# Performance work log

Measured on AMD Instinct MI355X. Metric: run time of the kernel, lower is better.

The kernel has to match this reference:

```python
import jax, jax.numpy as jnp
import numpy as np

B, N_NODES, VOCAB, H = 128, 1023, 2048, 256  # depth-9 perfect binary trees (heap layout)


def setup_inputs() -> dict:
    key = jax.random.key(0)
    k1, k2, k3, k4, k5 = jax.random.split(key, 5)
    tokens = jax.random.randint(k1, (B, N_NODES), 0, VOCAB)
    emb = jax.random.normal(k2, (VOCAB, H), dtype=jnp.float32) * 0.02
    Wx = jax.random.normal(k3, (H, 5 * H), dtype=jnp.float32) * 0.02
    Ul = jax.random.normal(k4, (H, 5 * H), dtype=jnp.float32) * 0.02
    Ur = jax.random.normal(k5, (H, 5 * H), dtype=jnp.float32) * 0.02
    b = jnp.zeros((5 * H,), dtype=jnp.float32)
    return {"tokens": tokens, "emb": emb, "Wx": Wx, "Ul": Ul, "Ur": Ur, "b": b}


def _tree_lstm(tokens, emb, Wx, Ul, Ur, b):
    # tokens: [B, 2^(D+1)-1] in level-order heap layout; children of heap index i
    # are 2i+1, 2i+2 -> within level d+1 they sit at offsets 2k, 2k+1.
    n_nodes = tokens.shape[1]
    depth = int(np.log2(n_nodes + 1)) - 1
    hdim = emb.shape[1]
    x_all = emb[tokens]  # [B, N, H] embedding lookup (memory-bound gather)
    h = c = None
    for d in range(depth, -1, -1):  # bottom-up over levels (fixed structural loop)
        start, n = 2 ** d - 1, 2 ** d
        x = x_all[:, start:start + n]  # [B, n, H]
        gates = jnp.einsum('bnh,hg->bng', x, Wx) + b
        if h is not None:
            hl, hr = h[:, 0::2], h[:, 1::2]
            cl, cr = c[:, 0::2], c[:, 1::2]
            gates = gates + jnp.einsum('bnh,hg->bng', hl, Ul) + jnp.einsum('bnh,hg->bng', hr, Ur)
        i, fl, fr, o, u = jnp.split(gates, 5, axis=-1)
        i, fl, fr, o = map(jax.nn.sigmoid, (i, fl, fr, o))
        u = jnp.tanh(u)
        c_new = i * u
        if c is not None:
            c_new = c_new + fl * cl + fr * cr
        c = c_new
        h = o * jnp.tanh(c)
    return h[:, 0], c[:, 0]  # root states, each [B, H]


def reference(tokens, emb, Wx, Ul, Ur, b):
    h_root, _ = _tree_lstm(tokens, emb, Wx, Ul, Ur, b)
    return h_root  # [B, H]
```

## Files before the change

kernel.cpp:

```cpp
#include <hip/hip_runtime.h>
#include <hip/hip_bf16.h>
#include <math.h>

#define B_SZ   128
#define HDIM   256
#define NG     1280
#define NNODES 1023
#define VOCAB  2048

typedef unsigned int uint32;
typedef short  short8v  __attribute__((ext_vector_type(8)));
typedef float  float4v  __attribute__((ext_vector_type(4)));

__device__ __forceinline__ float sigm(float x) {
    return 1.0f / (1.0f + __expf(-x));
}
__device__ __forceinline__ float tanh_fast(float x) {
    return 2.0f / (1.0f + __expf(-2.0f * x)) - 1.0f;
}
__device__ __forceinline__ float bf2f(unsigned short u) {
    return __uint_as_float(((uint32)u) << 16);
}
__device__ __forceinline__ unsigned short f2bf(float f) {
    uint32 x = __float_as_uint(f);
    uint32 r = (x + 0x7FFFu + ((x >> 16) & 1u)) >> 16;
    return (unsigned short)r;
}

__device__ __forceinline__ void dma16(const unsigned short* gptr, unsigned short* lptr) {
    __builtin_amdgcn_global_load_lds(
        (const __attribute__((address_space(1))) void*)gptr,
        (__attribute__((address_space(3))) void*)lptr, 16, 0, 0);
}

__global__ __launch_bounds__(256) void embb_kernel(
    const float* __restrict__ emb, unsigned short* __restrict__ embb)
{
    const int t = blockIdx.x * 256 + threadIdx.x;
    const float4 v0 = *(const float4*)(emb + (size_t)t * 8);
    const float4 v1 = *(const float4*)(emb + (size_t)t * 8 + 4);
    short8v o;
    o[0] = (short)f2bf(v0.x); o[1] = (short)f2bf(v0.y);
    o[2] = (short)f2bf(v0.z); o[3] = (short)f2bf(v0.w);
    o[4] = (short)f2bf(v1.x); o[5] = (short)f2bf(v1.y);
    o[6] = (short)f2bf(v1.z); o[7] = (short)f2bf(v1.w);
    *(short8v*)(embb + (size_t)t * 8) = o;
}

__global__ __launch_bounds__(256) void prep_wtf(
    const float* __restrict__ Ul, const float* __restrict__ Ur,
    const float* __restrict__ Wx, unsigned short* __restrict__ WTf)
{
    const int t = blockIdx.x * 256 + threadIdx.x;
    const int l = t & 63;
    const int q = l >> 4, c = l & 15;
    const int ks = (t >> 6) % 24;
    const int ng = t / (24 * 64);
    const int col = ng * 16 + c;
    const int k = ks * 32 + q * 8;
    const float* src = (k < 256) ? (Ul + (size_t)k * NG + col)
                     : (k < 512) ? (Ur + (size_t)(k - 256) * NG + col)
                                 : (Wx + (size_t)(k - 512) * NG + col);
    short8v v;
    #pragma unroll
    for (int j = 0; j < 8; ++j) v[j] = (short)f2bf(src[(size_t)j * NG]);
    *(short8v*)(WTf + (size_t)t * 8) = v;
}

__global__ __launch_bounds__(256, 2) void ewb_mfma(
    const unsigned short* __restrict__ WTf, const unsigned short* __restrict__ embb,
    const float* __restrict__ bias, unsigned short* __restrict__ EWb)
{
    __shared__ __align__(16) unsigned short Ab[2][4096];
    __shared__ __align__(16) unsigned short wbE[20480];

    const int tid  = threadIdx.x;
    const int lane = tid & 63;
    const int w    = tid >> 6;
    const int quad = lane >> 4, col15 = lane & 15;
    const int jt = blockIdx.x;
    const int rowBase = blockIdx.y * 64;
    const int jbase   = jt * 64;

    const unsigned short* agp[2];
    unsigned short* ldst[2];
    #pragma unroll
    for (int t = 0; t < 2; ++t) {
        const int ch = 2 * w + t, sub = ch >> 2, rt = ch & 3;
        const int srow = rowBase + rt * 16 + col15;
        agp[t]  = embb + (size_t)srow * HDIM + sub * 32 + quad * 8;
        ldst[t] = &Ab[0][0] + ch * 512;
    }

    const short8v* WTfv = (const short8v*)WTf;
    uint32 boff[5];
    #pragma unroll
    for (int g = 0; g < 5; ++g)
        boff[g] = ((g * 16 + jt * 4 + w) * 24 + 16) * 64 + lane;

    float4v acc[4][5];
    #pragma unroll
    for (int rt = 0; rt < 4; ++rt)
        #pragma unroll
        for (int g = 0; g < 5; ++g)
            #pragma unroll
            for (int e = 0; e < 4; ++e) acc[rt][g][e] = 0.0f;

    dma16(agp[0], ldst[0]); dma16(agp[1], ldst[1]);
    __syncthreads();

    #pragma unroll
    for (int s = 0; s < 4; ++s) {
        if (s < 3) {
            dma16(agp[0] + (s + 1) * 64, ldst[0] + ((s + 1) & 1) * 4096);
            dma16(agp[1] + (s + 1) * 64, ldst[1] + ((s + 1) & 1) * 4096);
        }
        #pragma unroll
        for (int sub = 0; sub < 2; ++sub) {
            short8v bf[5];
            #pragma unroll
            for (int g = 0; g < 5; ++g) bf[g] = WTfv[boff[g] + (s * 2 + sub) * 64];
            #pragma unroll
            for (int rt = 0; rt < 4; ++rt) {
                const short8v af = *(const short8v*)&Ab[s & 1][(sub * 4 + rt) * 512 + lane * 8];
                #pragma unroll
                for (int g = 0; g < 5; ++g)
                    acc[rt][g] = __builtin_amdgcn_mfma_f32_16x16x32_bf16(
                        af, bf[g], acc[rt][g], 0, 0, 0);
            }
        }
        __syncthreads();
    }

    const int jl = w * 16 + col15;
    const int j  = jbase + jl;
    float bz[5];
    #pragma unroll
    for (int g = 0; g < 5; ++g) bz[g] = bias[g * 256 + j];
    const int jchunk = jl >> 3, jpos = jl & 7;

    #pragma unroll
    for (int rt = 0; rt < 4; ++rt) {
        #pragma unroll
        for (int reg = 0; reg < 4; ++reg) {
            const int rr = rt * 16 + quad * 4 + reg;
            const int roff = ((jchunk + 2 * quad) & 7) * 8 + jpos;
            #pragma unroll
            for (int g = 0; g < 5; ++g)
                wbE[(g * 64 + rr) * 64 + roff] = f2bf(acc[rt][g][reg] + bz[g]);
        }
    }
    __syncthreads();

    #pragma unroll
    for (int k2 = 0; k2 < 10; ++k2) {
        const int c = tid + k2 * 256;
        const int g = c >> 9, rr = (c >> 3) & 63, u = c & 7;
        const int ru = (u + 2 * ((rr >> 2) & 3)) & 7;
        const short8v v = *(const short8v*)&wbE[(g * 64 + rr) * 64 + ru * 8];
        *(short8v*)(EWb + (size_t)(rowBase + rr) * NG + g * 256 + jbase + u * 8) = v;
    }
}

__global__ __launch_bounds__(256, 2) void leaf_kernel(
    const unsigned short* __restrict__ WTf, const unsigned short* __restrict__ embb,
    const float* __restrict__ bias, const int* __restrict__ tokens,
    unsigned short* __restrict__ hdst, unsigned short* __restrict__ cdst)
{
    __shared__ __align__(16) unsigned short Ab[2][4096];
    __shared__ __align__(16) unsigned short wb[2 * 4096];

    const int tid  = threadIdx.x;
    const int lane = tid & 63;
    const int w    = tid >> 6;
    const int quad = lane >> 4, col15 = lane & 15;
    const int jt = blockIdx.x;
    const int rowBase = blockIdx.y * 64;
    const int jbase   = jt * 64;

    const unsigned short* agp[2];
    unsigned short* ldst[2];
    #pragma unroll
    for (int t = 0; t < 2; ++t) {
        const int ch = 2 * w + t, sub = ch >> 2, rt = ch & 3;
        const int srow = rowBase + rt * 16 + col15;
        const int sb = srow >> 9, si = srow & 511;
        const int stok = tokens[sb * NNODES + 511 + si];
        agp[t]  = embb + (size_t)stok * HDIM + sub * 32 + quad * 8;
        ldst[t] = &Ab[0][0] + ch * 512;
    }

    const short8v* WTfv = (const short8v*)WTf;
    uint32 boff[3];
    boff[0] = ((0 * 16 + jt * 4 + w) * 24 + 16) * 64 + lane;
    boff[1] = ((3 * 16 + jt * 4 + w) * 24 + 16) * 64 + lane;
    boff[2] = ((4 * 16 + jt * 4 + w) * 24 + 16) * 64 + lane;

    float4v acc[4][3];
    #pragma unroll
    for (int rt = 0; rt < 4; ++rt)
        #pragma unroll
        for (int gi = 0; gi < 3; ++gi)
            #pragma unroll
            for (int e = 0; e < 4; ++e) acc[rt][gi][e] = 0.0f;

    dma16(agp[0], ldst[0]); dma16(agp[1], ldst[1]);
    __syncthreads();

    #pragma unroll
    for (int s = 0; s < 4; ++s) {
        if (s < 3) {
            dma16(agp[0] + (s + 1) * 64, ldst[0] + ((s + 1) & 1) * 4096);
            dma16(agp[1] + (s + 1) * 64, ldst[1] + ((s + 1) & 1) * 4096);
        }
        #pragma unroll
        for (int sub = 0; sub < 2; ++sub) {
            short8v bf[3];
            #pragma unroll
            for (int gi = 0; gi < 3; ++gi) bf[gi] = WTfv[boff[gi] + (s * 2 + sub) * 64];
            #pragma unroll
            for (int rt = 0; rt < 4; ++rt) {
                const short8v af = *(const short8v*)&Ab[s & 1][(sub * 4 + rt) * 512 + lane * 8];
                #pragma unroll
                for (int gi = 0; gi < 3; ++gi)
                    acc[rt][gi] = __builtin_amdgcn_mfma_f32_16x16x32_bf16(
                        af, bf[gi], acc[rt][gi], 0, 0, 0);
            }
        }
        __syncthreads();
    }

    const int jl = w * 16 + col15;
    const int j  = jbase + jl;
    const float b_i = bias[j], b_o = bias[768 + j], b_u = bias[1024 + j];
    const int jchunk = jl >> 3, jpos = jl & 7;

    #pragma unroll
    for (int rt = 0; rt < 4; ++rt) {
        #pragma unroll
        for (int reg = 0; reg < 4; ++reg) {
            const int rr = rt * 16 + quad * 4 + reg;
            const float gi = acc[rt][0][reg] + b_i;
            const float go = acc[rt][1][reg] + b_o;
            const float gu = acc[rt][2][reg] + b_u;
            const float c = sigm(gi) * tanh_fast(gu);
            const float h = sigm(go) * tanh_fast(c);
            const int roff = ((jchunk + 2 * quad) & 7) * 8 + jpos;
            wb[rr * 64 + roff]        = f2bf(h);
            wb[4096 + rr * 64 + roff] = f2bf(c);
        }
    }
    __syncthreads();
    #pragma unroll
    for (int k2 = 0; k2 < 4; ++k2) {
        const int c = tid + k2 * 256;
        const int arr = c >> 9, rr = (c >> 3) & 63, u = c & 7;
        const int ru = (u + 2 * ((rr >> 2) & 3)) & 7;
        const short8v v = *(const short8v*)(wb + (arr * 4096 + rr * 64 + ru * 8));
        unsigned short* dstp = (arr ? cdst : hdst) +
            (size_t)(rowBase + rr) * HDIM + jbase + u * 8;
        *(short8v*)dstp = v;
    }
}

__global__ __launch_bounds__(256, 2) void level_kernel(
    const unsigned short* __restrict__ WTf, const unsigned short* __restrict__ EWb,
    const int* __restrict__ tokens,
    const unsigned short* __restrict__ hsrc, const unsigned short* __restrict__ csrc,
    unsigned short* __restrict__ hdst, unsigned short* __restrict__ cdst,
    float* __restrict__ out, const int d)
{
    const int n = 1 << d;

    __shared__ __align__(16) unsigned short Ab[2][4096];
    __shared__ __align__(16) unsigned short ews[2560 * 8];
    __shared__ __align__(16) unsigned short cst[1024 * 8];

    const int tid  = threadIdx.x;
    const int lane = tid & 63;
    const int w    = tid >> 6;
    const int quad = lane >> 4, col15 = lane & 15;
    const int jt = blockIdx.x;
    const int rowBase = blockIdx.y * 64;
    const int jbase   = jt * 64;

    const unsigned short* agp[2];
    unsigned short* ldst[2];
    #pragma unroll
    for (int t = 0; t < 2; ++t) {
        const int ch = 2 * w + t, sub = ch >> 2, rt = ch & 3;
        const int srow = rowBase + rt * 16 + col15;
        agp[t]  = hsrc + (size_t)(2 * srow) * HDIM + sub * 32 + quad * 8;
        ldst[t] = &Ab[0][0] + ch * 512;
    }

    const short8v* WTfv = (const short8v*)WTf;
    uint32 boff[5];
    #pragma unroll
    for (int g = 0; g < 5; ++g)
        boff[g] = ((g * 16 + jt * 4 + w) * 24) * 64 + lane;

    float4v acc[4][5];
    #pragma unroll
    for (int rt = 0; rt < 4; ++rt)
        #pragma unroll
        for (int g = 0; g < 5; ++g)
            #pragma unroll
            for (int e = 0; e < 4; ++e) acc[rt][g][e] = 0.0f;

    dma16(agp[0], ldst[0]); dma16(agp[1], ldst[1]);
    __syncthreads();

    #pragma unroll
    for (int s = 0; s < 8; ++s) {
        if (s < 7) {
            dma16(agp[0] + (s + 1) * 64, ldst[0] + ((s + 1) & 1) * 4096);
            dma16(agp[1] + (s + 1) * 64, ldst[1] + ((s + 1) & 1) * 4096);
        }

        if (s >= 2 && s <= 6) {
            #pragma unroll
            for (int t2 = 0; t2 < 2; ++t2) {
                const int it = (s - 2) * 2 + t2;
                const int c = tid + it * 256;
                const uint32 row = (uint32)c / 40u;
                const int rem = c - (int)row * 40;
                const int g = rem >> 3, u = rem & 7;
                const int grow = rowBase + (int)row;
                const int tok = tokens[(grow >> d) * NNODES + (n - 1) + (grow & (n - 1))];
                dma16(EWb + (size_t)tok * NG + g * 256 + jbase + u * 8,
                      ews + ((size_t)it * 256 + w * 64) * 8);
            }
            if (s >= 5) {
                #pragma unroll
                for (int t2 = 0; t2 < 2; ++t2) {
                    const int k2 = (s - 5) * 2 + t2;
                    const int c = tid + k2 * 256;
                    const int rr = c >> 4, side = (c >> 3) & 1, u = c & 7;
                    dma16(csrc + (size_t)(2 * (rowBase + rr) + side) * HDIM + jbase + u * 8,
                          cst + ((size_t)k2 * 256 + w * 64) * 8);
                }
            }
        }

        #pragma unroll
        for (int sub = 0; sub < 2; ++sub) {
            short8v bf[5];
            #pragma unroll
            for (int g = 0; g < 5; ++g) bf[g] = WTfv[boff[g] + (s * 2 + sub) * 64];
            #pragma unroll
            for (int rt = 0; rt < 4; ++rt) {
                const short8v af = *(const short8v*)&Ab[s & 1][(sub * 4 + rt) * 512 + lane * 8];
                #pragma unroll
                for (int g = 0; g < 5; ++g)
                    acc[rt][g] = __builtin_amdgcn_mfma_f32_16x16x32_bf16(
                        af, bf[g], acc[rt][g], 0, 0, 0);
            }
        }
        __syncthreads();
    }

    const int jl = w * 16 + col15;
    const int j  = jbase + jl;
    float hv[4][4], cv[4][4];
    #pragma unroll
    for (int rt = 0; rt < 4; ++rt) {
        #pragma unroll
        for (int reg = 0; reg < 4; ++reg) {
            const int rr = rt * 16 + quad * 4 + reg;
            const float gi  = acc[rt][0][reg] + bf2f(ews[rr * 320 +       jl]);
            const float gfl = acc[rt][1][reg] + bf2f(ews[rr * 320 +  64 + jl]);
            const float gfr = acc[rt][2][reg] + bf2f(ews[rr * 320 + 128 + jl]);
            const float go  = acc[rt][3][reg] + bf2f(ews[rr * 320 + 192 + jl]);
            const float gu  = acc[rt][4][reg] + bf2f(ews[rr * 320 + 256 + jl]);
            const float cl  = bf2f(cst[rr * 128 +      jl]);
            const float cr  = bf2f(cst[rr * 128 + 64 + jl]);
            const float ii = sigm(gi), fl = sigm(gfl), fr = sigm(gfr), oo = sigm(go);
            const float uu = tanh_fast(gu);
            const float c = ii * uu + fl * cl + fr * cr;
            const float h = oo * tanh_fast(c);
            cv[rt][reg] = c; hv[rt][reg] = h;
            if (d == 0) out[(size_t)(rowBase + rr) * HDIM + j] = h;
        }
    }
    __syncthreads();

    const int jchunk = jl >> 3, jpos = jl & 7;
    #pragma unroll
    for (int rt = 0; rt < 4; ++rt) {
        #pragma unroll
        for (int reg = 0; reg < 4; ++reg) {
            const int rr = rt * 16 + quad * 4 + reg;
            const int roff = ((jchunk + 2 * quad) & 7) * 8 + jpos;
            ews[rr * 64 + roff]        = f2bf(hv[rt][reg]);
            ews[4096 + rr * 64 + roff] = f2bf(cv[rt][reg]);
        }
    }
    __syncthreads();
    #pragma unroll
    for (int k2 = 0; k2 < 4; ++k2) {
        const int c = tid + k2 * 256;
        const int arr = c >> 9, rr = (c >> 3) & 63, u = c & 7;
        const int ru = (u + 2 * ((rr >> 2) & 3)) & 7;
        const short8v v = *(const short8v*)(ews + (arr * 4096 + rr * 64 + ru * 8));
        unsigned short* dstp = (arr ? cdst : hdst) +
            (size_t)(rowBase + rr) * HDIM + jbase + u * 8;
        *(short8v*)dstp = v;
    }
}

extern "C" void kernel_launch(void* const* d_in, const int* in_sizes, int n_in,
                              void* d_out, int out_size, void* d_ws, size_t ws_size,
                              hipStream_t stream)
{
    const int*   tokens = (const int*)d_in[0];
    const float* emb    = (const float*)d_in[1];
    const float* Wx     = (const float*)d_in[2];
    const float* Ul     = (const float*)d_in[3];
    const float* Ur     = (const float*)d_in[4];
    const float* bias   = (const float*)d_in[5];
    float* out = (float*)d_out;

    const size_t EW_ELEMS  = (size_t)VOCAB * NG;
    const size_t EMB_ELEMS = (size_t)VOCAB * HDIM;
    const size_t WTF_ELEMS = (size_t)80 * 24 * 64 * 8;
    const size_t SLOT_A    = (size_t)512 * B_SZ * HDIM;
    const size_t SLOT_B    = (size_t)256 * B_SZ * HDIM;
    const size_t REQUIRED  = (EW_ELEMS + EMB_ELEMS + WTF_ELEMS + 2 * (SLOT_A + SLOT_B)) * 2;
    if (ws_size < REQUIRED || d_ws == nullptr) return;

    char* ws = (char*)d_ws;
    unsigned short* EWb  = (unsigned short*)ws;
    unsigned short* embb = EWb + EW_ELEMS;
    unsigned short* WTf  = embb + EMB_ELEMS;
    unsigned short* hA   = WTf + WTF_ELEMS;
    unsigned short* cA   = hA + SLOT_A;
    unsigned short* hB   = cA + SLOT_A;
    unsigned short* cB   = hB + SLOT_B;

    embb_kernel<<<dim3(256), 256, 0, stream>>>(emb, embb);
    prep_wtf<<<dim3(480), 256, 0, stream>>>(Ul, Ur, Wx, WTf);
    ewb_mfma<<<dim3(4, 32), 256, 0, stream>>>(WTf, embb, bias, EWb);

    leaf_kernel<<<dim3(4, 1024), 256, 0, stream>>>(WTf, embb, bias, tokens, hA, cA);

    for (int d = 8; d >= 0; --d) {
        const int NRB = 2 << d;
        const bool evenD = ((d & 1) == 0);
        const unsigned short* hs = evenD ? hA : hB;
        const unsigned short* cs = evenD ? cA : cB;
        unsigned short* hd = evenD ? hB : hA;
        unsigned short* cd = evenD ? cB : cA;
        level_kernel<<<dim3(4, NRB), 256, 0, stream>>>(
            WTf, EWb, tokens, hs, cs, hd, cd, out, d);
    }
}
```

Measured before the change: 370.0 us.

## Replace leaf GEMM with per-token leaf state table gathered at level 8

Leaf states depend only on the token, so h and c are computed once per vocabulary entry (2048 rows) from the precomputed token-gate table. This replaces the leaf MFMA kernel that ran over 65536 leaf rows. The level-8 kernel then gathers left and right child h and c from that table by token id instead of from a dense leaf buffer. This removes the leaf GEMM and its 65536-row writes, at the cost of indirect gathers and extra branching in the level kernel.

```diff
diff --git a/kernel.cpp b/kernel.cpp
--- a/kernel.cpp
+++ b/kernel.cpp
@@ -162,13 +162,34 @@
     }
 }
 
-__global__ __launch_bounds__(256, 2) void leaf_kernel(
-    const unsigned short* __restrict__ WTf, const unsigned short* __restrict__ embb,
-    const float* __restrict__ bias, const int* __restrict__ tokens,
-    unsigned short* __restrict__ hdst, unsigned short* __restrict__ cdst)
-{
+__global__ __launch_bounds__(256) void leaftab_kernel(
+    const unsigned short* __restrict__ EWb,
+    unsigned short* __restrict__ Hleaf, unsigned short* __restrict__ Cleaf)
+{
+    const int t = blockIdx.x * 256 + threadIdx.x;
+    const int tok = t >> 8, j = t & 255;
+    const float gi = bf2f(EWb[(size_t)tok * NG + j]);
+    const float go = bf2f(EWb[(size_t)tok * NG + 768 + j]);
+    const float gu = bf2f(EWb[(size_t)tok * NG + 1024 + j]);
+    const float c = sigm(gi) * tanh_fast(gu);
+    const float h = sigm(go) * tanh_fast(c);
+    Hleaf[t] = f2bf(h);
+    Cleaf[t] = f2bf(c);
+}
+
+__global__ __launch_bounds__(256, 2) void level_kernel(
+    const unsigned short* __restrict__ WTf, const unsigned short* __restrict__ EWb,
+    const int* __restrict__ tokens,
+    const unsigned short* __restrict__ Hleaf, const unsigned short* __restrict__ Cleaf,
+    const unsigned short* __restrict__ hsrc, const unsigned short* __restrict__ csrc,
+    unsigned short* __restrict__ hdst, unsigned short* __restrict__ cdst,
+    float* __restrict__ out, const int d)
+{
+    const int n = 1 << d;
+
     __shared__ __align__(16) unsigned short Ab[2][4096];
-    __shared__ __align__(16) unsigned short wb[2 * 4096];
+    __shared__ __align__(16) unsigned short ews[2560 * 8];
+    __shared__ __align__(16) unsigned short cst[1024 * 8];
 
     const int tid  = threadIdx.x;
     const int lane = tid & 63;
@@ -178,119 +199,23 @@
     const int rowBase = blockIdx.y * 64;
     const int jbase   = jt * 64;
 
-    const unsigned short* agp[2];
+    const unsigned short* agp_lo[2];
+    const unsigned short* agp_hi[2];
     unsigned short* ldst[2];
     #pragma unroll
     for (int t = 0; t < 2; ++t) {
         const int ch = 2 * w + t, sub = ch >> 2, rt = ch & 3;
         const int srow = rowBase + rt * 16 + col15;
-        const int sb = srow >> 9, si = srow & 511;
-        const int stok = tokens[sb * NNODES + 511 + si];
-        agp[t]  = embb + (size_t)stok * HDIM + sub * 32 + quad * 8;
-        ldst[t] = &Ab[0][0] + ch * 512;
-    }
-
-    const short8v* WTfv = (const short8v*)WTf;
-    uint32 boff[3];
-    boff[0] = ((0 * 16 + jt * 4 + w) * 24 + 16) * 64 + lane;
-    boff[1] = ((3 * 16 + jt * 4 + w) * 24 + 16) * 64 + lane;
-    boff[2] = ((4 * 16 + jt * 4 + w) * 24 + 16) * 64 + lane;
-
-    float4v acc[4][3];
-    #pragma unroll
-    for (int rt = 0; rt < 4; ++rt)
-        #pragma unroll
-        for (int gi = 0; gi < 3; ++gi)
-            #pragma unroll
-            for (int e = 0; e < 4; ++e) acc[rt][gi][e] = 0.0f;
-
-    dma16(agp[0], ldst[0]); dma16(agp[1], ldst[1]);
-    __syncthreads();
-
-    #pragma unroll
-    for (int s = 0; s < 4; ++s) {
-        if (s < 3) {
-            dma16(agp[0] + (s + 1) * 64, ldst[0] + ((s + 1) & 1) * 4096);
-            dma16(agp[1] + (s + 1) * 64, ldst[1] + ((s + 1) & 1) * 4096);
-        }
-        #pragma unroll
-        for (int sub = 0; sub < 2; ++sub) {
-            short8v bf[3];
-            #pragma unroll
-            for (int gi = 0; gi < 3; ++gi) bf[gi] = WTfv[boff[gi] + (s * 2 + sub) * 64];
-            #pragma unroll
-            for (int rt = 0; rt < 4; ++rt) {
-                const short8v af = *(const short8v*)&Ab[s & 1][(sub * 4 + rt) * 512 + lane * 8];
-                #pragma unroll
-                for (int gi = 0; gi < 3; ++gi)
-                    acc[rt][gi] = __builtin_amdgcn_mfma_f32_16x16x32_bf16(
-                        af, bf[gi], acc[rt][gi], 0, 0, 0);
-            }
-        }
-        __syncthreads();
-    }
-
-    const int jl = w * 16 + col15;
-    const int j  = jbase + jl;
-    const float b_i = bias[j], b_o = bias[768 + j], b_u = bias[1024 + j];
-    const int jchunk = jl >> 3, jpos = jl & 7;
-
-    #pragma unroll
-    for (int rt = 0; rt < 4; ++rt) {
-        #pragma unroll
-        for (int reg = 0; reg < 4; ++reg) {
-            const int rr = rt * 16 + quad * 4 + reg;
-            const float gi = acc[rt][0][reg] + b_i;
-            const float go = acc[rt][1][reg] + b_o;
-            const float gu = acc[rt][2][reg] + b_u;
-            const float c = sigm(gi) * tanh_fast(gu);
-            const float h = sigm(go) * tanh_fast(c);
-            const int roff = ((jchunk + 2 * quad) & 7) * 8 + jpos;
-            wb[rr * 64 + roff]        = f2bf(h);
-            wb[4096 + rr * 64 + roff] = f2bf(c);
-        }
-    }
-    __syncthreads();
-    #pragma unroll
-    for (int k2 = 0; k2 < 4; ++k2) {
-        const int c = tid + k2 * 256;
-        const int arr = c >> 9, rr = (c >> 3) & 63, u = c & 7;
-        const int ru = (u + 2 * ((rr >> 2) & 3)) & 7;
-        const short8v v = *(const short8v*)(wb + (arr * 4096 + rr * 64 + ru * 8));
-        unsigned short* dstp = (arr ? cdst : hdst) +
-            (size_t)(rowBase + rr) * HDIM + jbase + u * 8;
-        *(short8v*)dstp = v;
-    }
-}
-
-__global__ __launch_bounds__(256, 2) void level_kernel(
-    const unsigned short* __restrict__ WTf, const unsigned short* __restrict__ EWb,
-    const int* __restrict__ tokens,
-    const unsigned short* __restrict__ hsrc, const unsigned short* __restrict__ csrc,
-    unsigned short* __restrict__ hdst, unsigned short* __restrict__ cdst,
-    float* __restrict__ out, const int d)
-{
-    const int n = 1 << d;
-
-    __shared__ __align__(16) unsigned short Ab[2][4096];
-    __shared__ __align__(16) unsigned short ews[2560 * 8];
-    __shared__ __align__(16) unsigned short cst[1024 * 8];
-
-    const int tid  = threadIdx.x;
-    const int lane = tid & 63;
-    const int w    = tid >> 6;
-    const int quad = lane >> 4, col15 = lane & 15;
-    const int jt = blockIdx.x;
-    const int rowBase = blockIdx.y * 64;
-    const int jbase   = jt * 64;
-
-    const unsigned short* agp[2];
-    unsigned short* ldst[2];
-    #pragma unroll
-    for (int t = 0; t < 2; ++t) {
-        const int ch = 2 * w + t, sub = ch >> 2, rt = ch & 3;
-        const int srow = rowBase + rt * 16 + col15;
-        agp[t]  = hsrc + (size_t)(2 * srow) * HDIM + sub * 32 + quad * 8;
+        if (d == 8) {
+            const int b = srow >> 8, i = srow & 255;
+            const int tokL = tokens[b * NNODES + 511 + 2 * i];
+            const int tokR = tokens[b * NNODES + 512 + 2 * i];
+            agp_lo[t] = Hleaf + (size_t)tokL * HDIM + sub * 32 + quad * 8;
+            agp_hi[t] = Hleaf + (size_t)tokR * HDIM + sub * 32 + quad * 8;
+        } else {
+            agp_lo[t] = hsrc + (size_t)(2 * srow) * HDIM + sub * 32 + quad * 8;
+            agp_hi[t] = agp_lo[t] + HDIM;
+        }
         ldst[t] = &Ab[0][0] + ch * 512;
     }
 
@@ -308,14 +233,19 @@
             #pragma unroll
             for (int e = 0; e < 4; ++e) acc[rt][g][e] = 0.0f;
 
-    dma16(agp[0], ldst[0]); dma16(agp[1], ldst[1]);
+    dma16(agp_lo[0], ldst[0]); dma16(agp_lo[1], ldst[1]);
     __syncthreads();
 
     #pragma unroll
     for (int s = 0; s < 8; ++s) {
         if (s < 7) {
-            dma16(agp[0] + (s + 1) * 64, ldst[0] + ((s + 1) & 1) * 4096);
-            dma16(agp[1] + (s + 1) * 64, ldst[1] + ((s + 1) & 1) * 4096);
+            const int sn = s + 1;
+            #pragma unroll
+            for (int t = 0; t < 2; ++t) {
+                const unsigned short* p = (sn < 4) ? (agp_lo[t] + sn * 64)
+                                                   : (agp_hi[t] + (sn - 4) * 64);
+                dma16(p, ldst[t] + (sn & 1) * 4096);
+            }
         }
 
         if (s >= 2 && s <= 6) {
@@ -337,8 +267,16 @@
                     const int k2 = (s - 5) * 2 + t2;
                     const int c = tid + k2 * 256;
                     const int rr = c >> 4, side = (c >> 3) & 1, u = c & 7;
-                    dma16(csrc + (size_t)(2 * (rowBase + rr) + side) * HDIM + jbase + u * 8,
-                          cst + ((size_t)k2 * 256 + w * 64) * 8);
+                    const unsigned short* src;
+                    if (d == 8) {
+                        const int grow = rowBase + rr;
+                        const int b = grow >> 8, i = grow & 255;
+                        const int tok = tokens[b * NNODES + 511 + 2 * i + side];
+                        src = Cleaf + (size_t)tok * HDIM + jbase + u * 8;
+                    } else {
+                        src = csrc + (size_t)(2 * (rowBase + rr) + side) * HDIM + jbase + u * 8;
+                    }
+                    dma16(src, cst + ((size_t)k2 * 256 + w * 64) * 8);
                 }
             }
         }
@@ -424,25 +362,28 @@
     const size_t EW_ELEMS  = (size_t)VOCAB * NG;
     const size_t EMB_ELEMS = (size_t)VOCAB * HDIM;
     const size_t WTF_ELEMS = (size_t)80 * 24 * 64 * 8;
-    const size_t SLOT_A    = (size_t)512 * B_SZ * HDIM;
-    const size_t SLOT_B    = (size_t)256 * B_SZ * HDIM;
-    const size_t REQUIRED  = (EW_ELEMS + EMB_ELEMS + WTF_ELEMS + 2 * (SLOT_A + SLOT_B)) * 2;
+    const size_t LT_ELEMS  = (size_t)VOCAB * HDIM;
+    const size_t SLOT_A    = (size_t)16384 * HDIM;
+    const size_t SLOT_B    = (size_t)32768 * HDIM;
+    const size_t REQUIRED  = (EW_ELEMS + EMB_ELEMS + WTF_ELEMS + 2 * LT_ELEMS
+                              + 2 * (SLOT_A + SLOT_B)) * 2;
     if (ws_size < REQUIRED || d_ws == nullptr) return;
 
     char* ws = (char*)d_ws;
-    unsigned short* EWb  = (unsigned short*)ws;
-    unsigned short* embb = EWb + EW_ELEMS;
-    unsigned short* WTf  = embb + EMB_ELEMS;
-    unsigned short* hA   = WTf + WTF_ELEMS;
-    unsigned short* cA   = hA + SLOT_A;
-    unsigned short* hB   = cA + SLOT_A;
-    unsigned short* cB   = hB + SLOT_B;
+    unsigned short* EWb   = (unsigned short*)ws;
+    unsigned short* embb  = EWb + EW_ELEMS;
+    unsigned short* WTf   = embb + EMB_ELEMS;
+    unsigned short* Hleaf = WTf + WTF_ELEMS;
+    unsigned short* Cleaf = Hleaf + LT_ELEMS;
+    unsigned short* hA    = Cleaf + LT_ELEMS;
+    unsigned short* cA    = hA + SLOT_A;
+    unsigned short* hB    = cA + SLOT_A;
+    unsigned short* cB    = hB + SLOT_B;
 
     embb_kernel<<<dim3(256), 256, 0, stream>>>(emb, embb);
     prep_wtf<<<dim3(480), 256, 0, stream>>>(Ul, Ur, Wx, WTf);
     ewb_mfma<<<dim3(4, 32), 256, 0, stream>>>(WTf, embb, bias, EWb);
-
-    leaf_kernel<<<dim3(4, 1024), 256, 0, stream>>>(WTf, embb, bias, tokens, hA, cA);
+    leaftab_kernel<<<dim3(2048), 256, 0, stream>>>(EWb, Hleaf, Cleaf);
 
     for (int d = 8; d >= 0; --d) {
         const int NRB = 2 << d;
@@ -452,6 +393,6 @@
         unsigned short* hd = evenD ? hB : hA;
         unsigned short* cd = evenD ? cB : cA;
         level_kernel<<<dim3(4, NRB), 256, 0, stream>>>(
-            WTf, EWb, tokens, hs, cs, hd, cd, out, d);
-    }
-}
+            WTf, EWb, tokens, Hleaf, Cleaf, hs, cs, hd, cd, out, d);
+    }
+}
```

New measurement: 340.5 us. 8.0% less time.
